# Kernel optimization log

Measured on AMD Instinct MI355X. Metric: run time of the kernel, lower is better.

The kernel has to match this reference:

```python
import jax, jax.numpy as jnp
import numpy as np

B, HOR, L, A, HID = 4096, 32, 512, 64, 1024


def _linear_params(key, fan_in, fan_out):
    kw, kb = jax.random.split(key)
    bound = 1.0 / np.sqrt(fan_in)
    W = jax.random.uniform(kw, (fan_in, fan_out), jnp.float32, -bound, bound)
    b = jax.random.uniform(kb, (fan_out,), jnp.float32, -bound, bound)
    return W, b


def setup_inputs() -> dict:
    key = jax.random.key(0)
    ks = jax.random.split(key, 11)
    initial_state = jax.random.normal(ks[0], (B, L), jnp.float32)
    action_sequence = jax.random.normal(ks[1], (B, HOR, A), jnp.float32)
    Wae, bae = _linear_params(ks[2], A, A)
    Wt1, bt1 = _linear_params(ks[3], L + A, HID)
    Wt2, bt2 = _linear_params(ks[4], HID, HID)
    Wt3, bt3 = _linear_params(ks[5], HID, L)
    Wo1, bo1 = _linear_params(ks[6], L, HID)
    Wo2, bo2 = _linear_params(ks[7], HID, L)
    Wh1, bh1 = _linear_params(ks[8], L + A, HID)
    Wh2, bh2 = _linear_params(ks[9], HID, 1)
    return dict(initial_state=initial_state, action_sequence=action_sequence,
                Wae=Wae, bae=bae, Wt1=Wt1, bt1=bt1, Wt2=Wt2, bt2=bt2,
                Wt3=Wt3, bt3=bt3, Wo1=Wo1, bo1=bo1, Wo2=Wo2, bo2=bo2,
                Wh1=Wh1, bh1=bh1, Wh2=Wh2, bh2=bh2)


def reference(initial_state, action_sequence, Wae, bae, Wt1, bt1, Wt2, bt2,
              Wt3, bt3, Wo1, bo1, Wo2, bo2, Wh1, bh1, Wh2, bh2):
    # rollout: sequential scan over horizon steps
    def step(state, action):
        # harm predictor on raw (state, action)
        sa = jnp.concatenate([state, action], axis=-1)            # [B, L+A]
        harm = jax.nn.sigmoid(jax.nn.relu(sa @ Wh1 + bh1) @ Wh2 + bh2)  # [B,1]
        # observation predictor on current state
        obs = jax.nn.relu(state @ Wo1 + bo1) @ Wo2 + bo2          # [B, L]
        # transition on (state, encoded action); residual update
        ae = action @ Wae + bae                                   # [B, A]
        sae = jnp.concatenate([state, ae], axis=-1)               # [B, L+A]
        h = jax.nn.relu(sae @ Wt1 + bt1)
        h = jax.nn.relu(h @ Wt2 + bt2)
        next_state = state + h @ Wt3 + bt3                        # [B, L]
        return next_state, (next_state, obs, harm[:, 0])

    actions_t = jnp.swapaxes(action_sequence, 0, 1)               # [HOR, B, A]
    _, (states_t, obs_t, harm_t) = jax.lax.scan(step, initial_state, actions_t)
    # states: initial + all next states -> [B, HOR+1, L]
    states = jnp.concatenate([initial_state[:, None, :],
                              jnp.swapaxes(states_t, 0, 1)], axis=1)
    observations = jnp.swapaxes(obs_t, 0, 1)                      # [B, HOR, L]
    harm_predictions = jnp.swapaxes(harm_t, 0, 1)                 # [B, HOR]
    return states, observations, harm_predictions
```

## Files before the change

### kernel.cpp

```cpp
#include <hip/hip_runtime.h>
#include <math.h>

#define B_ 4096
#define HOR_ 32
#define L_ 512
#define A_ 64
#define HID_ 1024

#define CB 512
#define MC (CB * HOR_)

typedef unsigned short ushort_t;
typedef __attribute__((ext_vector_type(4))) float f32x4;
typedef __attribute__((ext_vector_type(8))) short s16x8;
typedef __attribute__((ext_vector_type(4))) short s16x4;
typedef __attribute__((ext_vector_type(8))) _Float16 f16x8;

__device__ __forceinline__ unsigned short bf16_rne(float x) {
    unsigned u = __builtin_bit_cast(unsigned, x);
    u += 0x7fffu + ((u >> 16) & 1u);
    return (unsigned short)(u >> 16);
}
__device__ __forceinline__ float bf16_to_f32(unsigned short h) {
    unsigned u = ((unsigned)h) << 16;
    return __builtin_bit_cast(float, u);
}

__device__ __forceinline__ int xcd_swz(int bid, int nwg) {
    return (bid & 7) * (nwg >> 3) + (bid >> 3);
}

template <int BMT, bool TWOSRC, bool SPLIT_OUT, bool RELU, bool RESID, bool F32OUT>
__global__ __launch_bounds__(512, 4) void trans_gemm(
    const _Float16* __restrict__ Ahi, const _Float16* __restrict__ Alo,
    int lda, int K,
    const float* __restrict__ Aae, int lda_ae, int aoff,
    const _Float16* __restrict__ Whi, const _Float16* __restrict__ Wlo,
    const float* __restrict__ bias,
    const float* __restrict__ resid, int ldr,
    _Float16* __restrict__ Ohi, _Float16* __restrict__ Olo, int ldoh,
    float* __restrict__ Of, int ldof)
{
    __shared__ _Float16 Ah[2][BMT][40];
    __shared__ _Float16 Al[2][BMT][40];
    __shared__ _Float16 Bh[2][64][40];
    __shared__ _Float16 Bl[2][64][40];

    const int gx = gridDim.x;
    const int bid = xcd_swz(blockIdx.y * gx + blockIdx.x, gx * gridDim.y);
    const int m0 = (bid / gx) * BMT;
    const int n0 = (bid % gx) * 64;

    const int tid = threadIdx.x;
    const int w = tid >> 6, l = tid & 63;
    const int wr = w >> 1, wc = w & 1;
    const int kg = l >> 4, lr = l & 15;
    constexpr int AF = BMT / 64;

    const int srow = tid >> 2, sg = tid & 3;
    const bool doA = (BMT == 128) || (tid < 256);
    const bool doB = (tid < 256);

    f32x4 acc[AF][2] = {};
    f16x8 rAh, rAl, rBh, rBl;

    const _Float16* pBh = Whi + (size_t)(n0 + (doB ? srow : 0)) * K + sg * 8;
    const _Float16* pBl = Wlo + (size_t)(n0 + (doB ? srow : 0)) * K + sg * 8;
    const _Float16* pAh = Ahi + (size_t)(m0 + (doA ? srow : 0)) * lda + sg * 8;
    const _Float16* pAl = Alo + (size_t)(m0 + (doA ? srow : 0)) * lda + sg * 8;
    const float* pAe = TWOSRC
        ? (Aae + (size_t)(m0 + (doA ? srow : 0)) * lda_ae + aoff + sg * 8)
        : nullptr;

    auto load_regs = [&](int ks) {
        const int k0 = ks * 32;
        if (doB) {
            rBh = *reinterpret_cast<const f16x8*>(pBh + k0);
            rBl = *reinterpret_cast<const f16x8*>(pBl + k0);
        }
        if (doA) {
            if (!TWOSRC || k0 < L_) {
                rAh = *reinterpret_cast<const f16x8*>(pAh + k0);
                rAl = *reinterpret_cast<const f16x8*>(pAl + k0);
            } else {
                const float* s = pAe + (k0 - L_);
                float4 v0 = *reinterpret_cast<const float4*>(s);
                float4 v1 = *reinterpret_cast<const float4*>(s + 4);
                float vv[8] = {v0.x, v0.y, v0.z, v0.w, v1.x, v1.y, v1.z, v1.w};
                f16x8 h, lo;
#pragma unroll
                for (int j = 0; j < 8; ++j) {
                    _Float16 hh = (_Float16)vv[j];
                    h[j] = hh;
                    lo[j] = (_Float16)(vv[j] - (float)hh);
                }
                rAh = h; rAl = lo;
            }
        }
    };
    auto write_lds = [&](int buf) {
        if (doB) {
            *reinterpret_cast<f16x8*>(&Bh[buf][srow][sg * 8]) = rBh;
            *reinterpret_cast<f16x8*>(&Bl[buf][srow][sg * 8]) = rBl;
        }
        if (doA) {
            *reinterpret_cast<f16x8*>(&Ah[buf][srow][sg * 8]) = rAh;
            *reinterpret_cast<f16x8*>(&Al[buf][srow][sg * 8]) = rAl;
        }
    };

    const int NT = K / 32;
    load_regs(0);
    write_lds(0);
    __syncthreads();
    int cur = 0;

    for (int ks = 0; ks < NT; ++ks) {
        if (ks + 1 < NT) load_regs(ks + 1);

        f16x8 ah[AF], al[AF], bh[2], bl[2];
#pragma unroll
        for (int i = 0; i < AF; ++i) {
            int r = wr * (BMT / 4) + i * 16 + lr;
            ah[i] = *reinterpret_cast<const f16x8*>(&Ah[cur][r][kg * 8]);
            al[i] = *reinterpret_cast<const f16x8*>(&Al[cur][r][kg * 8]);
        }
#pragma unroll
        for (int j = 0; j < 2; ++j) {
            int r = wc * 32 + j * 16 + lr;
            bh[j] = *reinterpret_cast<const f16x8*>(&Bh[cur][r][kg * 8]);
            bl[j] = *reinterpret_cast<const f16x8*>(&Bl[cur][r][kg * 8]);
        }
#pragma unroll
        for (int i = 0; i < AF; ++i)
#pragma unroll
            for (int j = 0; j < 2; ++j) {
                acc[i][j] = __builtin_amdgcn_mfma_f32_16x16x32_f16(
                    ah[i], bh[j], acc[i][j], 0, 0, 0);
                acc[i][j] = __builtin_amdgcn_mfma_f32_16x16x32_f16(
                    ah[i], bl[j], acc[i][j], 0, 0, 0);
                acc[i][j] = __builtin_amdgcn_mfma_f32_16x16x32_f16(
                    al[i], bh[j], acc[i][j], 0, 0, 0);
            }

        if (ks + 1 < NT) {
            write_lds(cur ^ 1);
            __syncthreads();
            cur ^= 1;
        }
    }

    float bv[2];
#pragma unroll
    for (int j = 0; j < 2; ++j) bv[j] = bias[n0 + wc * 32 + j * 16 + lr];

#pragma unroll
    for (int i = 0; i < AF; ++i)
#pragma unroll
        for (int j = 0; j < 2; ++j)
#pragma unroll
            for (int r = 0; r < 4; ++r) {
                int row = m0 + wr * (BMT / 4) + i * 16 + kg * 4 + r;
                int col = n0 + wc * 32 + j * 16 + lr;
                float v = acc[i][j][r] + bv[j];
                if (RESID)
                    v += resid[(size_t)row * ldr + col];
                if (RELU) v = fmaxf(v, 0.f);
                if (F32OUT)
                    Of[(size_t)row * ldof + col] = v;
                if (SPLIT_OUT) {
                    _Float16 h = (_Float16)v;
                    Ohi[(size_t)row * ldoh + col] = h;
                    Olo[(size_t)row * ldoh + col] = (_Float16)(v - (float)h);
                }
            }
}

__global__ __launch_bounds__(256) void split_transpose(
    const float* __restrict__ W, _Float16* __restrict__ Whi,
    _Float16* __restrict__ Wlo, int K, int N)
{
    int k = blockIdx.x * 256 + threadIdx.x;
    int n = blockIdx.y;
    if (k < K) {
        float v = W[(size_t)k * N + n];
        _Float16 h = (_Float16)v;
        Whi[(size_t)n * K + k] = h;
        Wlo[(size_t)n * K + k] = (_Float16)(v - (float)h);
    }
}

__global__ __launch_bounds__(256) void ae_all(
    const float* __restrict__ actions,
    const float* __restrict__ Wae,
    const float* __restrict__ bae,
    float* __restrict__ ae)
{
    const long r = (long)blockIdx.x * 4 + (threadIdx.x >> 6);
    const int c = threadIdx.x & 63;
    const float* arow = actions + r * 64;
    float acc = bae[c];
#pragma unroll 16
    for (int k = 0; k < 64; ++k) acc = fmaf(arow[k], Wae[k * 64 + c], acc);
    ae[r * 64 + c] = acc;
}

__global__ __launch_bounds__(256) void ae_step(
    const float* __restrict__ actions, const float* __restrict__ Wae,
    const float* __restrict__ bae, int t, float* __restrict__ aeS)
{
    const long b = (long)blockIdx.x * 4 + (threadIdx.x >> 6);
    const int c = threadIdx.x & 63;
    const float* arow = actions + (b * HOR_ + t) * 64;
    float acc = bae[c];
#pragma unroll 16
    for (int k = 0; k < 64; ++k) acc = fmaf(arow[k], Wae[k * 64 + c], acc);
    aeS[b * 64 + c] = acc;
}

__global__ __launch_bounds__(256) void init_split(
    const float* __restrict__ init, float* __restrict__ states,
    _Float16* __restrict__ sth, _Float16* __restrict__ stl)
{
    size_t i = (size_t)blockIdx.x * 256 + threadIdx.x;
    size_t b = i >> 9, l = i & 511;
    float v = init[i];
    states[b * (33 * L_) + l] = v;
    _Float16 h = (_Float16)v;
    sth[i] = h;
    stl[i] = (_Float16)(v - (float)h);
}


__global__ __launch_bounds__(256) void cast_transpose(
    const float* __restrict__ W, ushort_t* __restrict__ WT, int K, int N)
{
    int k = blockIdx.x * 256 + threadIdx.x;
    int n = blockIdx.y;
    if (k < K) WT[(long)n * K + k] = bf16_rne(W[(long)k * N + n]);
}

__global__ __launch_bounds__(256) void mm_split(
    const float* __restrict__ Astate,
    const float* __restrict__ Aact,
    int Ktot,
    const ushort_t* __restrict__ WT,
    int N,
    const float* __restrict__ bias,
    ushort_t* __restrict__ Out)
{
    __shared__ ushort_t Ahi[128][40];
    __shared__ ushort_t Alo[128][40];
    __shared__ ushort_t Bt[128][40];

    const int tid = threadIdx.x;
    const int gx = gridDim.x;
    const int bid = xcd_swz(blockIdx.y * gx + blockIdx.x, gx * gridDim.y);
    const int m0 = (bid / gx) * 128;
    const int n0 = (bid % gx) * 128;
    const int w = tid >> 6;
    const int l = tid & 63;
    const int wm = w >> 1, wn = w & 1;
    const int kg = l >> 4, lr = l & 15;

    f32x4 acc[4][4] = {};

    for (int k0 = 0; k0 < Ktot; k0 += 32) {
#pragma unroll
        for (int s = 0; s < 4; ++s) {
            int idx = tid + s * 256;
            int arow = idx >> 3;
            int ch = idx & 7;
            int m = m0 + arow;
            const float* src;
            if (k0 < L_) {
                src = Astate + (long)((m >> 5) * 33 + (m & 31)) * L_ + k0 + ch * 4;
            } else {
                src = Aact + (long)m * A_ + (k0 - L_) + ch * 4;
            }
            float4 v = *reinterpret_cast<const float4*>(src);
            unsigned short h0 = bf16_rne(v.x), h1 = bf16_rne(v.y),
                           h2 = bf16_rne(v.z), h3 = bf16_rne(v.w);
            unsigned short e0 = bf16_rne(v.x - bf16_to_f32(h0));
            unsigned short e1 = bf16_rne(v.y - bf16_to_f32(h1));
            unsigned short e2 = bf16_rne(v.z - bf16_to_f32(h2));
            unsigned short e3 = bf16_rne(v.w - bf16_to_f32(h3));
            s16x4 hv = {(short)h0, (short)h1, (short)h2, (short)h3};
            s16x4 lv = {(short)e0, (short)e1, (short)e2, (short)e3};
            *reinterpret_cast<s16x4*>(&Ahi[arow][ch * 4]) = hv;
            *reinterpret_cast<s16x4*>(&Alo[arow][ch * 4]) = lv;
        }
#pragma unroll
        for (int s = 0; s < 2; ++s) {
            int idx = tid + s * 256;
            int brow = idx >> 2;
            int ch = idx & 3;
            s16x8 wv = *reinterpret_cast<const s16x8*>(
                &WT[(long)(n0 + brow) * Ktot + k0 + ch * 8]);
            *reinterpret_cast<s16x8*>(&Bt[brow][ch * 8]) = wv;
        }
        __syncthreads();

        s16x8 ah[4], al[4], bb[4];
#pragma unroll
        for (int i = 0; i < 4; ++i) {
            int r = wm * 64 + i * 16 + lr;
            ah[i] = *reinterpret_cast<const s16x8*>(&Ahi[r][kg * 8]);
            al[i] = *reinterpret_cast<const s16x8*>(&Alo[r][kg * 8]);
        }
#pragma unroll
        for (int j = 0; j < 4; ++j) {
            int r = wn * 64 + j * 16 + lr;
            bb[j] = *reinterpret_cast<const s16x8*>(&Bt[r][kg * 8]);
        }
#pragma unroll
        for (int i = 0; i < 4; ++i)
#pragma unroll
            for (int j = 0; j < 4; ++j) {
                acc[i][j] = __builtin_amdgcn_mfma_f32_16x16x32_bf16(
                    ah[i], bb[j], acc[i][j], 0, 0, 0);
                acc[i][j] = __builtin_amdgcn_mfma_f32_16x16x32_bf16(
                    al[i], bb[j], acc[i][j], 0, 0, 0);
            }
        __syncthreads();
    }

    float bv[4];
#pragma unroll
    for (int j = 0; j < 4; ++j) bv[j] = bias[n0 + wn * 64 + j * 16 + lr];
#pragma unroll
    for (int i = 0; i < 4; ++i)
#pragma unroll
        for (int j = 0; j < 4; ++j)
#pragma unroll
            for (int r = 0; r < 4; ++r) {
                int row = m0 + wm * 64 + i * 16 + kg * 4 + r;
                int col = n0 + wn * 64 + j * 16 + lr;
                float v = fmaxf(acc[i][j][r] + bv[j], 0.f);
                Out[(long)row * N + col] = bf16_rne(v);
            }
}

__global__ __launch_bounds__(256) void mm_bf16(
    const ushort_t* __restrict__ Abf,
    const ushort_t* __restrict__ WT,
    int N,
    const float* __restrict__ bias,
    float* __restrict__ Out)
{
    __shared__ ushort_t At[128][40];
    __shared__ ushort_t Bt[128][40];

    const int tid = threadIdx.x;
    const int gx = gridDim.x;
    const int bid = xcd_swz(blockIdx.y * gx + blockIdx.x, gx * gridDim.y);
    const int m0 = (bid / gx) * 128;
    const int n0 = (bid % gx) * 128;
    const int w = tid >> 6;
    const int l = tid & 63;
    const int wm = w >> 1, wn = w & 1;
    const int kg = l >> 4, lr = l & 15;

    f32x4 acc[4][4] = {};

    for (int k0 = 0; k0 < HID_; k0 += 32) {
#pragma unroll
        for (int s = 0; s < 2; ++s) {
            int idx = tid + s * 256;
            int arow = idx >> 2;
            int ch = idx & 3;
            s16x8 av = *reinterpret_cast<const s16x8*>(
                &Abf[(long)(m0 + arow) * HID_ + k0 + ch * 8]);
            *reinterpret_cast<s16x8*>(&At[arow][ch * 8]) = av;
        }
#pragma unroll
        for (int s = 0; s < 2; ++s) {
            int idx = tid + s * 256;
            int brow = idx >> 2;
            int ch = idx & 3;
            s16x8 wv = *reinterpret_cast<const s16x8*>(
                &WT[(long)(n0 + brow) * HID_ + k0 + ch * 8]);
            *reinterpret_cast<s16x8*>(&Bt[brow][ch * 8]) = wv;
        }
        __syncthreads();

        s16x8 aa[4], bb[4];
#pragma unroll
        for (int i = 0; i < 4; ++i)
            aa[i] = *reinterpret_cast<const s16x8*>(&At[wm * 64 + i * 16 + lr][kg * 8]);
#pragma unroll
        for (int j = 0; j < 4; ++j)
            bb[j] = *reinterpret_cast<const s16x8*>(&Bt[wn * 64 + j * 16 + lr][kg * 8]);
#pragma unroll
        for (int i = 0; i < 4; ++i)
#pragma unroll
            for (int j = 0; j < 4; ++j)
                acc[i][j] = __builtin_amdgcn_mfma_f32_16x16x32_bf16(
                    aa[i], bb[j], acc[i][j], 0, 0, 0);
        __syncthreads();
    }

    float bv[4];
#pragma unroll
    for (int j = 0; j < 4; ++j) bv[j] = bias[n0 + wn * 64 + j * 16 + lr];
#pragma unroll
    for (int i = 0; i < 4; ++i)
#pragma unroll
        for (int j = 0; j < 4; ++j)
#pragma unroll
            for (int r = 0; r < 4; ++r) {
                int row = m0 + wm * 64 + i * 16 + kg * 4 + r;
                int col = n0 + wn * 64 + j * 16 + lr;
                Out[(long)row * N + col] = acc[i][j][r] + bv[j];
            }
}

__global__ __launch_bounds__(256) void harm_reduce(
    const ushort_t* __restrict__ hh,
    const float* __restrict__ Wh2,
    const float* __restrict__ bh2,
    float* __restrict__ harm)
{
    const int wave = threadIdx.x >> 6;
    const int lane = threadIdx.x & 63;
    const long r = (long)blockIdx.x * 4 + wave;
    const ushort_t* row = hh + r * HID_;
    float s = 0.f;
#pragma unroll
    for (int q = 0; q < 2; ++q) {
        s16x8 a = *reinterpret_cast<const s16x8*>(&row[lane * 16 + q * 8]);
        float4 w0 = *reinterpret_cast<const float4*>(&Wh2[lane * 16 + q * 8]);
        float4 w1 = *reinterpret_cast<const float4*>(&Wh2[lane * 16 + q * 8 + 4]);
        s = fmaf(bf16_to_f32((unsigned short)a[0]), w0.x, s);
        s = fmaf(bf16_to_f32((unsigned short)a[1]), w0.y, s);
        s = fmaf(bf16_to_f32((unsigned short)a[2]), w0.z, s);
        s = fmaf(bf16_to_f32((unsigned short)a[3]), w0.w, s);
        s = fmaf(bf16_to_f32((unsigned short)a[4]), w1.x, s);
        s = fmaf(bf16_to_f32((unsigned short)a[5]), w1.y, s);
        s = fmaf(bf16_to_f32((unsigned short)a[6]), w1.z, s);
        s = fmaf(bf16_to_f32((unsigned short)a[7]), w1.w, s);
    }
#pragma unroll
    for (int off = 32; off; off >>= 1) s += __shfl_down(s, off);
    if (lane == 0) {
        float x = s + bh2[0];
        harm[r] = 1.f / (1.f + expf(-x));
    }
}

extern "C" void kernel_launch(void* const* d_in, const int* in_sizes, int n_in,
                              void* d_out, int out_size, void* d_ws, size_t ws_size,
                              hipStream_t stream)
{
    const float* initial = (const float*)d_in[0];
    const float* actions = (const float*)d_in[1];
    const float* Wae = (const float*)d_in[2];
    const float* bae = (const float*)d_in[3];
    const float* Wt1 = (const float*)d_in[4];
    const float* bt1 = (const float*)d_in[5];
    const float* Wt2 = (const float*)d_in[6];
    const float* bt2 = (const float*)d_in[7];
    const float* Wt3 = (const float*)d_in[8];
    const float* bt3 = (const float*)d_in[9];
    const float* Wo1 = (const float*)d_in[10];
    const float* bo1 = (const float*)d_in[11];
    const float* Wo2 = (const float*)d_in[12];
    const float* bo2 = (const float*)d_in[13];
    const float* Wh1 = (const float*)d_in[14];
    const float* bh1 = (const float*)d_in[15];
    const float* Wh2 = (const float*)d_in[16];
    const float* bh2 = (const float*)d_in[17];

    float* out = (float*)d_out;
    float* states = out;
    float* obs = out + (size_t)B_ * 33 * L_;
    float* harm = obs + (size_t)B_ * HOR_ * L_;

    char* wsb = (char*)d_ws;
    size_t off = 0;
    auto alloc = [&](size_t bytes) { char* q = wsb + off; off += bytes; return q; };
    ushort_t* WT_o1 = (ushort_t*)alloc((size_t)HID_ * L_ * 2);
    ushort_t* WT_o2 = (ushort_t*)alloc((size_t)L_ * HID_ * 2);
    ushort_t* WT_h1 = (ushort_t*)alloc((size_t)HID_ * 576 * 2);
    _Float16* Wt1h = (_Float16*)alloc((size_t)HID_ * 576 * 2);
    _Float16* Wt1l = (_Float16*)alloc((size_t)HID_ * 576 * 2);
    _Float16* Wt2h = (_Float16*)alloc((size_t)HID_ * HID_ * 2);
    _Float16* Wt2l = (_Float16*)alloc((size_t)HID_ * HID_ * 2);
    _Float16* Wt3h = (_Float16*)alloc((size_t)L_ * HID_ * 2);
    _Float16* Wt3l = (_Float16*)alloc((size_t)L_ * HID_ * 2);
    _Float16* sth  = (_Float16*)alloc((size_t)B_ * L_ * 2);
    _Float16* stl  = (_Float16*)alloc((size_t)B_ * L_ * 2);
    _Float16* h1h  = (_Float16*)alloc((size_t)B_ * HID_ * 2);
    _Float16* h1l  = (_Float16*)alloc((size_t)B_ * HID_ * 2);
    _Float16* h2h  = (_Float16*)alloc((size_t)B_ * HID_ * 2);
    _Float16* h2l  = (_Float16*)alloc((size_t)B_ * HID_ * 2);
    float* ae = (float*)alloc(0);
    const size_t need_batched = off + (size_t)B_ * HOR_ * A_ * 4;
    const bool batched_ae = (ws_size >= need_batched);

    ushort_t* oh = (ushort_t*)h1h;

    cast_transpose<<<dim3(2, HID_), 256, 0, stream>>>(Wo1, WT_o1, L_, HID_);
    cast_transpose<<<dim3(4, L_), 256, 0, stream>>>(Wo2, WT_o2, HID_, L_);
    cast_transpose<<<dim3(3, HID_), 256, 0, stream>>>(Wh1, WT_h1, 576, HID_);
    split_transpose<<<dim3(3, HID_), 256, 0, stream>>>(Wt1, Wt1h, Wt1l, 576, HID_);
    split_transpose<<<dim3(4, HID_), 256, 0, stream>>>(Wt2, Wt2h, Wt2l, HID_, HID_);
    split_transpose<<<dim3(4, L_), 256, 0, stream>>>(Wt3, Wt3h, Wt3l, HID_, L_);

    init_split<<<(B_ * L_) / 256, 256, 0, stream>>>(initial, states, sth, stl);
    if (batched_ae)
        ae_all<<<(B_ * HOR_) / 4, 256, 0, stream>>>(actions, Wae, bae, ae);

    const int ldS = 33 * L_;
    const int lda_ae = batched_ae ? (HOR_ * A_) : A_;

    for (int t = 0; t < HOR_; ++t) {
        if (!batched_ae)
            ae_step<<<B_ / 4, 256, 0, stream>>>(actions, Wae, bae, t, ae);
        const int aoff = batched_ae ? t * A_ : 0;
        trans_gemm<128, true, true, true, false, false>
            <<<dim3(HID_ / 64, B_ / 128), 512, 0, stream>>>(
            sth, stl, L_, 576, ae, lda_ae, aoff,
            Wt1h, Wt1l, bt1, nullptr, 0, h1h, h1l, HID_, nullptr, 0);
        trans_gemm<128, false, true, true, false, false>
            <<<dim3(HID_ / 64, B_ / 128), 512, 0, stream>>>(
            h1h, h1l, HID_, HID_, nullptr, 0, 0,
            Wt2h, Wt2l, bt2, nullptr, 0, h2h, h2l, HID_, nullptr, 0);
        trans_gemm<64, false, true, false, true, true>
            <<<dim3(L_ / 64, B_ / 64), 512, 0, stream>>>(
            h2h, h2l, HID_, HID_, nullptr, 0, 0,
            Wt3h, Wt3l, bt3, states + (size_t)t * L_, ldS,
            sth, stl, L_, states + (size_t)(t + 1) * L_, ldS);
    }

    for (int c = 0; c < B_ / CB; ++c) {
        const float* Sc = states + (size_t)c * CB * 33 * L_;
        const float* Ac = actions + (size_t)c * CB * HOR_ * A_;
        mm_split<<<dim3(HID_ / 128, MC / 128), 256, 0, stream>>>(
            Sc, nullptr, L_, WT_o1, HID_, bo1, oh);
        mm_bf16<<<dim3(L_ / 128, MC / 128), 256, 0, stream>>>(
            oh, WT_o2, L_, bo2, obs + (size_t)c * CB * HOR_ * L_);
        mm_split<<<dim3(HID_ / 128, MC / 128), 256, 0, stream>>>(
            Sc, Ac, 576, WT_h1, HID_, bh1, oh);
        harm_reduce<<<MC / 4, 256, 0, stream>>>(
            oh, Wh2, bh2, harm + (size_t)c * CB * HOR_);
    }
}
```

Baseline: 4.197 ms.

## Stage GEMM tiles via direct global-to-LDS loads instead of register staging

Replaces the register round-trip (global load into VGPRs, then LDS store) with global_load_lds 16-byte direct transfers into the double-buffered tiles. The LDS padding is dropped so each lane's destination is contiguous, as the direct-load addressing requires. For the BMT=64 variant, B-tile loading moves to the upper half of the threads to balance issue work. The fp32 action-encoding slice is still loaded into registers, split into hi/lo halves, and stored manually. The aim is to cut VGPR pressure and instruction count in the main loop. The risks are LDS bank conflicts from the unpadded layout and relying on the compiler to insert the right waits before the barrier.

```diff
diff --git a/kernel.cpp b/kernel.cpp
--- a/kernel.cpp
+++ b/kernel.cpp
@@ -28,6 +28,12 @@
 
 __device__ __forceinline__ int xcd_swz(int bid, int nwg) {
     return (bid & 7) * (nwg >> 3) + (bid >> 3);
+}
+
+__device__ __forceinline__ void gld16(const void* g, void* l) {
+    __builtin_amdgcn_global_load_lds(
+        (const __attribute__((address_space(1))) void*)g,
+        (__attribute__((address_space(3))) void*)l, 16, 0, 0);
 }
 
 template <int BMT, bool TWOSRC, bool SPLIT_OUT, bool RELU, bool RESID, bool F32OUT>
@@ -41,10 +47,10 @@
     _Float16* __restrict__ Ohi, _Float16* __restrict__ Olo, int ldoh,
     float* __restrict__ Of, int ldof)
 {
-    __shared__ _Float16 Ah[2][BMT][40];
-    __shared__ _Float16 Al[2][BMT][40];
-    __shared__ _Float16 Bh[2][64][40];
-    __shared__ _Float16 Bl[2][64][40];
+    __shared__ _Float16 Ah[2][BMT][32];
+    __shared__ _Float16 Al[2][BMT][32];
+    __shared__ _Float16 Bh[2][64][32];
+    __shared__ _Float16 Bl[2][64][32];
 
     const int gx = gridDim.x;
     const int bid = xcd_swz(blockIdx.y * gx + blockIdx.x, gx * gridDim.y);
@@ -57,66 +63,52 @@
     const int kg = l >> 4, lr = l & 15;
     constexpr int AF = BMT / 64;
 
-    const int srow = tid >> 2, sg = tid & 3;
     const bool doA = (BMT == 128) || (tid < 256);
-    const bool doB = (tid < 256);
+    const bool doB = (BMT == 128) ? (tid < 256) : (tid >= 256);
+    const int srowA = tid >> 2;
+    const int srowB = (BMT == 128) ? (tid >> 2) : ((tid - 256) >> 2);
+    const int sg = tid & 3;
 
     f32x4 acc[AF][2] = {};
-    f16x8 rAh, rAl, rBh, rBl;
-
-    const _Float16* pBh = Whi + (size_t)(n0 + (doB ? srow : 0)) * K + sg * 8;
-    const _Float16* pBl = Wlo + (size_t)(n0 + (doB ? srow : 0)) * K + sg * 8;
-    const _Float16* pAh = Ahi + (size_t)(m0 + (doA ? srow : 0)) * lda + sg * 8;
-    const _Float16* pAl = Alo + (size_t)(m0 + (doA ? srow : 0)) * lda + sg * 8;
+    float4 e0, e1;
+
+    const _Float16* pAh = Ahi + (size_t)(m0 + srowA) * lda + sg * 8;
+    const _Float16* pAl = Alo + (size_t)(m0 + srowA) * lda + sg * 8;
+    const _Float16* pBh = Whi + (size_t)(n0 + srowB) * K + sg * 8;
+    const _Float16* pBl = Wlo + (size_t)(n0 + srowB) * K + sg * 8;
     const float* pAe = TWOSRC
-        ? (Aae + (size_t)(m0 + (doA ? srow : 0)) * lda_ae + aoff + sg * 8)
+        ? (Aae + (size_t)(m0 + srowA) * lda_ae + aoff + sg * 8 - L_)
         : nullptr;
 
-    auto load_regs = [&](int ks) {
+    auto stage = [&](int buf, int ks) {
         const int k0 = ks * 32;
         if (doB) {
-            rBh = *reinterpret_cast<const f16x8*>(pBh + k0);
-            rBl = *reinterpret_cast<const f16x8*>(pBl + k0);
-        }
-        if (doA) {
-            if (!TWOSRC || k0 < L_) {
-                rAh = *reinterpret_cast<const f16x8*>(pAh + k0);
-                rAl = *reinterpret_cast<const f16x8*>(pAl + k0);
-            } else {
-                const float* s = pAe + (k0 - L_);
-                float4 v0 = *reinterpret_cast<const float4*>(s);
-                float4 v1 = *reinterpret_cast<const float4*>(s + 4);
-                float vv[8] = {v0.x, v0.y, v0.z, v0.w, v1.x, v1.y, v1.z, v1.w};
-                f16x8 h, lo;
-#pragma unroll
-                for (int j = 0; j < 8; ++j) {
-                    _Float16 hh = (_Float16)vv[j];
-                    h[j] = hh;
-                    lo[j] = (_Float16)(vv[j] - (float)hh);
-                }
-                rAh = h; rAl = lo;
-            }
+            gld16(pBh + k0, &Bh[buf][srowB][sg * 8]);
+            gld16(pBl + k0, &Bl[buf][srowB][sg * 8]);
+        }
+        if (doA && (!TWOSRC || k0 < L_)) {
+            gld16(pAh + k0, &Ah[buf][srowA][sg * 8]);
+            gld16(pAl + k0, &Al[buf][srowA][sg * 8]);
         }
     };
-    auto write_lds = [&](int buf) {
-        if (doB) {
-            *reinterpret_cast<f16x8*>(&Bh[buf][srow][sg * 8]) = rBh;
-            *reinterpret_cast<f16x8*>(&Bl[buf][srow][sg * 8]) = rBl;
-        }
-        if (doA) {
-            *reinterpret_cast<f16x8*>(&Ah[buf][srow][sg * 8]) = rAh;
-            *reinterpret_cast<f16x8*>(&Al[buf][srow][sg * 8]) = rAl;
-        }
-    };
 
     const int NT = K / 32;
-    load_regs(0);
-    write_lds(0);
+    stage(0, 0);
     __syncthreads();
     int cur = 0;
 
     for (int ks = 0; ks < NT; ++ks) {
-        if (ks + 1 < NT) load_regs(ks + 1);
+        const bool havepf = (ks + 1 < NT);
+        const int k0n = (ks + 1) * 32;
+        const bool aeNext = TWOSRC && havepf && (k0n >= L_);
+
+        if (havepf) {
+            stage(cur ^ 1, ks + 1);
+            if (aeNext && doA) {
+                e0 = *reinterpret_cast<const float4*>(pAe + k0n);
+                e1 = *reinterpret_cast<const float4*>(pAe + k0n + 4);
+            }
+        }
 
         f16x8 ah[AF], al[AF], bh[2], bl[2];
 #pragma unroll
@@ -143,8 +135,19 @@
                     al[i], bh[j], acc[i][j], 0, 0, 0);
             }
 
-        if (ks + 1 < NT) {
-            write_lds(cur ^ 1);
+        if (havepf) {
+            if (aeNext && doA) {
+                float vv[8] = {e0.x, e0.y, e0.z, e0.w, e1.x, e1.y, e1.z, e1.w};
+                f16x8 h, lo;
+#pragma unroll
+                for (int j = 0; j < 8; ++j) {
+                    _Float16 hh = (_Float16)vv[j];
+                    h[j] = hh;
+                    lo[j] = (_Float16)(vv[j] - (float)hh);
+                }
+                *reinterpret_cast<f16x8*>(&Ah[cur ^ 1][srowA][sg * 8]) = h;
+                *reinterpret_cast<f16x8*>(&Al[cur ^ 1][srowA][sg * 8]) = lo;
+            }
             __syncthreads();
             cur ^= 1;
         }
```

Result: faster. 3.924 ms (-6.5%).
